# Kernel tuning notes

Measured on AMD Instinct MI355X. Metric: run time of the kernel, lower is better.

## Reference

```python
import jax, jax.numpy as jnp
import numpy as np

ALPHA = 0.1
BETA = 1.1
NUM_CLASSES = 16
EPS = 1e-8  # matches torch cosine_similarity eps
BATCH = 131072
DIM = 512


def setup_inputs() -> dict:
    key = jax.random.key(0)
    k1, k2 = jax.random.split(key)
    embeddings = jax.random.normal(k1, (BATCH, DIM), dtype=jnp.float32)
    labels = jax.random.randint(k2, (BATCH,), 0, NUM_CLASSES)
    return {"embeddings": embeddings, "labels": labels}


def _cos_dist(a, b):
    # a: [M, D], b: [N, D] -> 1 - cosine_similarity, shape [M, N]
    an = a / jnp.maximum(jnp.linalg.norm(a, axis=-1, keepdims=True), EPS)
    bn = b / jnp.maximum(jnp.linalg.norm(b, axis=-1, keepdims=True), EPS)
    return 1.0 - an @ bn.T


def reference(embeddings, labels):
    C = NUM_CLASSES
    N = embeddings.shape[0]
    dt = embeddings.dtype

    # class centroids (dummy anchors) via scatter-mean
    cnt = jax.ops.segment_sum(jnp.ones((N,), dt), labels, num_segments=C)  # [C]
    sums = jax.ops.segment_sum(embeddings, labels, num_segments=C)        # [C, D]
    centroids = sums / jnp.maximum(cnt, 1.0)[:, None]
    present = cnt > 0

    # close class pairs: i < j, both present, centroid distance <= beta
    pd = _cos_dist(centroids, centroids)                    # [C, C]
    upper = jnp.triu(jnp.ones((C, C), bool), k=1)
    pairmask = upper & (pd <= BETA) & present[:, None] & present[None, :]
    pm = pairmask.astype(dt)
    deg = pm.sum(1) + pm.sum(0)                             # pairs involving each class

    # distances from every centroid to every sample
    D = _cos_dist(centroids, embeddings)                    # [C, N]

    # intra: each sample of class c contributes relu(d(cent_c, x) - alpha),
    # once per close pair involving c
    d_own = D[labels, jnp.arange(N)]                        # [N]
    intra_sum = jnp.sum(deg[labels] * jax.nn.relu(d_own - ALPHA))

    # inter: S[c, c'] = sum over samples with label c' of relu(beta - d(cent_c, x))
    S = jax.ops.segment_sum(jax.nn.relu(BETA - D).T, labels, num_segments=C).T  # [C, C]
    inter_sum = jnp.sum(pm * (S + S.T))

    # number of terms in each loss list: sum over pairs of (cnt_i + cnt_j)
    count = jnp.sum(deg * cnt)
    denom = jnp.maximum(count, 1.0)
    num_pairs = pm.sum()

    loss = jnp.where(num_pairs > 0, intra_sum / denom + inter_sum / denom, 0.0)
    return loss
```

## Files before the change

### kernel.cpp

```cpp
#include <hip/hip_runtime.h>

constexpr float kAlpha = 0.1f;
constexpr float kBeta  = 1.1f;
constexpr int   kC     = 16;
constexpr int   kD     = 512;
constexpr float kEps   = 1e-8f;

constexpr int SUMS_OFF = 0;
constexpr int CNT_OFF  = 8192;
constexpr int TOT_OFF  = 8208;
constexpr int CTR1_OFF = 8209;
constexpr int CTR2_OFF = 8210;
constexpr int FLAG_OFF = 8224;
constexpr int PDM_OFF  = 8960;
constexpr int CN_OFF   = 9216;
constexpr int MSK_OFF  = 17408;
constexpr int SCL_OFF  = 17424;
constexpr int ZERO_FLOATS = 8211;

__device__ __forceinline__ float dot4(float4 a, float4 b) {
    return a.x * b.x + a.y * b.y + a.z * b.z + a.w * b.w;
}

__global__ __launch_bounds__(256) void k1_sums(const float* __restrict__ emb,
                                               const int* __restrict__ labels,
                                               float* __restrict__ ws,
                                               int N, int rpb) {
    __shared__ float lacc[kC * kD];
    float* sums  = ws + SUMS_OFF;
    float* cnt_g = ws + CNT_OFF;
    float* cn_g  = ws + CN_OFF;
    float* pdm_g = ws + PDM_OFF;
    float* scal  = ws + SCL_OFF;
    unsigned* mask_g = (unsigned*)(ws + MSK_OFF);
    int* ctr1 = (int*)(ws + CTR1_OFF);
    int* flag = (int*)(ws + FLAG_OFF);

    int tid = threadIdx.x;
    int wave = tid >> 6, lane = tid & 63;
    int half = wave & 1, strm = wave >> 1;

    for (int i = tid; i < kC * kD; i += 256) lacc[i] = 0.f;

    float4 acc[kC];
#pragma unroll
    for (int c = 0; c < kC; ++c) acc[c] = make_float4(0.f, 0.f, 0.f, 0.f);
    float cacc = 0.f;

    const float4* e4 = (const float4*)emb;
    int r0 = blockIdx.x * rpb;
    int r1 = min(r0 + rpb, N);
    const int o = half * 64 + lane;

    for (int base = r0 + strm; base < r1; base += 8) {
        int rA = base;
        int rB = base + 2, rC = base + 4, rD = base + 6;
        int cB = rB < r1 ? rB : rA;
        int cC = rC < r1 ? rC : rA;
        int cD = rD < r1 ? rD : rA;
        float4 xA = e4[(size_t)rA * 128 + o];
        float4 xB = e4[(size_t)cB * 128 + o];
        float4 xC = e4[(size_t)cC * 128 + o];
        float4 xD = e4[(size_t)cD * 128 + o];
        int laA = __builtin_amdgcn_readfirstlane(labels[rA]);
        int laB = rB < r1 ? __builtin_amdgcn_readfirstlane(labels[cB]) : -1;
        int laC = rC < r1 ? __builtin_amdgcn_readfirstlane(labels[cC]) : -1;
        int laD = rD < r1 ? __builtin_amdgcn_readfirstlane(labels[cD]) : -1;
#pragma unroll
        for (int c = 0; c < kC; ++c) {
            float mA = (laA == c) ? 1.f : 0.f;
            float mB = (laB == c) ? 1.f : 0.f;
            float mC = (laC == c) ? 1.f : 0.f;
            float mD = (laD == c) ? 1.f : 0.f;
            acc[c].x += mA * xA.x; acc[c].y += mA * xA.y; acc[c].z += mA * xA.z; acc[c].w += mA * xA.w;
            acc[c].x += mB * xB.x; acc[c].y += mB * xB.y; acc[c].z += mB * xB.z; acc[c].w += mB * xB.w;
            acc[c].x += mC * xC.x; acc[c].y += mC * xC.y; acc[c].z += mC * xC.z; acc[c].w += mC * xC.w;
            acc[c].x += mD * xD.x; acc[c].y += mD * xD.y; acc[c].z += mD * xD.z; acc[c].w += mD * xD.w;
        }
        if (half == 0) {
            cacc += ((laA == lane) ? 1.f : 0.f) + ((laB == lane) ? 1.f : 0.f)
                  + ((laC == lane) ? 1.f : 0.f) + ((laD == lane) ? 1.f : 0.f);
        }
    }

    __syncthreads();
#pragma unroll 1
    for (int s = 0; s < kC; ++s) {
        int c = (s + wave * 4) & 15;
        float* p = &lacc[c * kD + half * 256 + lane];
        float4 a = acc[c];
        p[0]   += a.x;
        p[64]  += a.y;
        p[128] += a.z;
        p[192] += a.w;
        __syncthreads();
    }

    for (int g = tid; g < kC * kD; g += 256) {
        int c = g >> 9, d = g & 511;
        int hh = d >> 8, u = d & 255;
        int l = u >> 2, k = u & 3;
        atomicAdd(&sums[g], lacc[c * kD + hh * 256 + k * 64 + l]);
    }
    if (half == 0 && lane < kC) atomicAdd(&cnt_g[lane], cacc);

    __threadfence();
    __syncthreads();
    if (tid == 0) {
        int old = atomicAdd(ctr1, 1);
        flag[blockIdx.x] = (old == (int)gridDim.x - 1) ? 1 : 0;
    }
    __syncthreads();
    if (flag[blockIdx.x] == 0) return;
    __threadfence();

    int c = tid >> 4, sub = tid & 15;
    float cntc = atomicAdd(&cnt_g[c], 0.f);
    float invc = 1.f / fmaxf(cntc, 1.f);
    float sq = 0.f;
    for (int d = sub; d < kD; d += 16) {
        float v = atomicAdd(&sums[c * kD + d], 0.f) * invc;
        lacc[c * kD + d] = v;
        sq += v * v;
    }
#pragma unroll
    for (int m = 1; m < 16; m <<= 1) sq += __shfl_xor(sq, m, 64);
    float inv = 1.f / fmaxf(sqrtf(sq), kEps);
    for (int d = sub; d < kD; d += 16) {
        float v = lacc[c * kD + d] * inv;
        lacc[c * kD + d] = v;
        cn_g[c * kD + d] = v;
    }
    __syncthreads();

    int pi = tid >> 4, pj = tid & 15;
    float dot = 0.f;
    for (int dd = 0; dd < kD; ++dd) {
        int d = (dd + tid) & (kD - 1);
        dot += lacc[pi * kD + d] * lacc[pj * kD + d];
    }
    pdm_g[tid] = 1.f - dot;
    __syncthreads();

    if (tid == 0) {
        float lc[kC];
        for (int a = 0; a < kC; ++a) lc[a] = atomicAdd(&cnt_g[a], 0.f);
        unsigned m[kC];
        for (int a = 0; a < kC; ++a) m[a] = 0u;
        float npairs = 0.f;
        for (int a = 0; a < kC; ++a)
            for (int b = a + 1; b < kC; ++b) {
                bool close = (pdm_g[a * kC + b] <= kBeta) && (lc[a] > 0.f) && (lc[b] > 0.f);
                if (close) { m[a] |= 1u << b; m[b] |= 1u << a; npairs += 1.f; }
            }
        float count = 0.f;
        for (int a = 0; a < kC; ++a) {
            mask_g[a] = m[a];
            count += (float)__popc(m[a]) * lc[a];
        }
        scal[0] = fmaxf(count, 1.f);
        scal[1] = npairs;
    }
}

__global__ __launch_bounds__(512, 2) void k3_main(const float* __restrict__ emb,
                                                  const int* __restrict__ labels,
                                                  float* __restrict__ ws,
                                                  float* __restrict__ out,
                                                  int N, int rpb) {
    __shared__ unsigned lmask[kC];
    __shared__ float wsum[8];
    const float* cn_g = ws + CN_OFF;
    const unsigned* mask_g = (const unsigned*)(ws + MSK_OFF);
    float* total = ws + TOT_OFF;
    const float* scal = ws + SCL_OFF;
    int* ctr2 = (int*)(ws + CTR2_OFF);

    int tid = threadIdx.x;
    int wave = tid >> 6, lane = tid & 63;
    int g = lane >> 4, j = lane & 15;

    const float4* w4 = (const float4*)cn_g;
    float4 wreg[4][8];
#pragma unroll
    for (int c = 0; c < 4; ++c)
#pragma unroll
        for (int i = 0; i < 8; ++i)
            wreg[c][i] = w4[(4 * g + c) * 128 + i * 16 + j];
    if (tid < kC) lmask[tid] = mask_g[tid];
    __syncthreads();

    int r0 = blockIdx.x * rpb;
    int r1 = min(r0 + rpb, N);
    const float4* src = (const float4*)emb;
    float priv = 0.f;

#define K3_COMPUTE(X, LAB)                                                     \
    do {                                                                       \
        float d0 = 0.f, d1 = 0.f, d2 = 0.f, d3 = 0.f, nrm = 0.f;               \
        _Pragma("unroll")                                                      \
        for (int i = 0; i < 8; ++i) {                                          \
            float4 x = X[i];                                                   \
            nrm += dot4(x, x);                                                 \
            d0 += dot4(x, wreg[0][i]);                                         \
            d1 += dot4(x, wreg[1][i]);                                         \
            d2 += dot4(x, wreg[2][i]);                                         \
            d3 += dot4(x, wreg[3][i]);                                         \
        }                                                                      \
        _Pragma("unroll")                                                      \
        for (int m = 1; m < 16; m <<= 1) {                                     \
            d0 += __shfl_xor(d0, m, 64);                                       \
            d1 += __shfl_xor(d1, m, 64);                                       \
            d2 += __shfl_xor(d2, m, 64);                                       \
            d3 += __shfl_xor(d3, m, 64);                                       \
            nrm += __shfl_xor(nrm, m, 64);                                     \
        }                                                                      \
        if (j == 0) {                                                          \
            unsigned mm = lmask[LAB];                                          \
            float inv = 1.f / fmaxf(sqrtf(nrm), kEps);                         \
            float dv[4] = {d0, d1, d2, d3};                                    \
            float s = 0.f;                                                     \
            _Pragma("unroll")                                                  \
            for (int c = 0; c < 4; ++c) {                                      \
                int cg = 4 * g + c;                                            \
                float dd = 1.f - dv[c] * inv;                                  \
                if ((mm >> cg) & 1u) s += fmaxf(kBeta - dd, 0.f);              \
                if (cg == LAB) s += (float)__popc(mm) * fmaxf(dd - kAlpha, 0.f);\
            }                                                                  \
            priv += s;                                                         \
        }                                                                      \
    } while (0)

    int rA = r0 + wave;
    if (rA < r1) {
        float4 xA[8], xB[8];
        int laA, laB;
#pragma unroll
        for (int i = 0; i < 8; ++i) xA[i] = src[(size_t)rA * 128 + i * 16 + j];
        laA = labels[rA];
        int rB = rA + 8;
        while (true) {
            bool vB = rB < r1;
            int rBi = vB ? rB : rA;
#pragma unroll
            for (int i = 0; i < 8; ++i) xB[i] = src[(size_t)rBi * 128 + i * 16 + j];
            laB = labels[rBi];
            K3_COMPUTE(xA, laA);
            if (!vB) break;

            int rN = rB + 8;
            bool vN = rN < r1;
            int rNi = vN ? rN : rB;
#pragma unroll
            for (int i = 0; i < 8; ++i) xA[i] = src[(size_t)rNi * 128 + i * 16 + j];
            laA = labels[rNi];
            K3_COMPUTE(xB, laB);
            if (!vN) break;
            rA = rN;
            rB = rN + 8;
        }
    }
#undef K3_COMPUTE

#pragma unroll
    for (int off = 32; off > 0; off >>= 1) priv += __shfl_down(priv, off, 64);
    if (lane == 0) wsum[wave] = priv;
    __syncthreads();
    if (tid == 0) {
        float t = 0.f;
#pragma unroll
        for (int w = 0; w < 8; ++w) t += wsum[w];
        atomicAdd(total, t);
        __threadfence();
        int old = atomicAdd(ctr2, 1);
        if (old == (int)gridDim.x - 1) {
            float tot = atomicAdd(total, 0.f);
            out[0] = (scal[1] > 0.f) ? (tot / scal[0]) : 0.f;
        }
    }
}

extern "C" void kernel_launch(void* const* d_in, const int* in_sizes, int n_in,
                              void* d_out, int out_size, void* d_ws, size_t ws_size,
                              hipStream_t stream) {
    const float* emb = (const float*)d_in[0];
    const int* labels = (const int*)d_in[1];
    int N = in_sizes[0] / kD;

    float* ws = (float*)d_ws;
    hipMemsetAsync(d_ws, 0, ZERO_FLOATS * sizeof(float), stream);

    int blocks1 = 512;
    int rpb1 = (N + blocks1 - 1) / blocks1;
    k1_sums<<<blocks1, 256, 0, stream>>>(emb, labels, ws, N, rpb1);

    int blocks3 = 256;
    int rpb3 = (N + blocks3 - 1) / blocks3;
    k3_main<<<blocks3, 512, 0, stream>>>(emb, labels, ws, (float*)d_out, N, rpb3);
}
```

Baseline: 559.0 us.

## Deepen load pipelining in both passes and double k1 block size

The centroid-sum kernel now runs 512 threads per block, and each wave loads 8 rows per iteration instead of 4, so more memory requests are in flight. The last-block flag moves from global memory into shared memory. The distance kernel switches from double buffering to a three-buffer rotation, keeping two row loads outstanding while one row is computed. The cost is higher register pressure, from the 16 float4 accumulators plus 8 row buffers in k1 and 24 float4 buffers in k3, which may limit occupancy.

Result: slower. 841.3 us (+50.5%).

```diff
diff --git a/kernel.cpp b/kernel.cpp
--- a/kernel.cpp
+++ b/kernel.cpp
@@ -11,7 +11,6 @@
 constexpr int TOT_OFF  = 8208;
 constexpr int CTR1_OFF = 8209;
 constexpr int CTR2_OFF = 8210;
-constexpr int FLAG_OFF = 8224;
 constexpr int PDM_OFF  = 8960;
 constexpr int CN_OFF   = 9216;
 constexpr int MSK_OFF  = 17408;
@@ -22,11 +21,12 @@
     return a.x * b.x + a.y * b.y + a.z * b.z + a.w * b.w;
 }
 
-__global__ __launch_bounds__(256) void k1_sums(const float* __restrict__ emb,
-                                               const int* __restrict__ labels,
-                                               float* __restrict__ ws,
-                                               int N, int rpb) {
+__global__ __launch_bounds__(512, 4) void k1_sums(const float* __restrict__ emb,
+                                                  const int* __restrict__ labels,
+                                                  float* __restrict__ ws,
+                                                  int N, int rpb) {
     __shared__ float lacc[kC * kD];
+    __shared__ int lastblk;
     float* sums  = ws + SUMS_OFF;
     float* cnt_g = ws + CNT_OFF;
     float* cn_g  = ws + CN_OFF;
@@ -34,13 +34,12 @@
     float* scal  = ws + SCL_OFF;
     unsigned* mask_g = (unsigned*)(ws + MSK_OFF);
     int* ctr1 = (int*)(ws + CTR1_OFF);
-    int* flag = (int*)(ws + FLAG_OFF);
 
     int tid = threadIdx.x;
     int wave = tid >> 6, lane = tid & 63;
     int half = wave & 1, strm = wave >> 1;
 
-    for (int i = tid; i < kC * kD; i += 256) lacc[i] = 0.f;
+    for (int i = tid; i < kC * kD; i += 512) lacc[i] = 0.f;
 
     float4 acc[kC];
 #pragma unroll
@@ -52,41 +51,41 @@
     int r1 = min(r0 + rpb, N);
     const int o = half * 64 + lane;
 
-    for (int base = r0 + strm; base < r1; base += 8) {
-        int rA = base;
-        int rB = base + 2, rC = base + 4, rD = base + 6;
-        int cB = rB < r1 ? rB : rA;
-        int cC = rC < r1 ? rC : rA;
-        int cD = rD < r1 ? rD : rA;
-        float4 xA = e4[(size_t)rA * 128 + o];
-        float4 xB = e4[(size_t)cB * 128 + o];
-        float4 xC = e4[(size_t)cC * 128 + o];
-        float4 xD = e4[(size_t)cD * 128 + o];
-        int laA = __builtin_amdgcn_readfirstlane(labels[rA]);
-        int laB = rB < r1 ? __builtin_amdgcn_readfirstlane(labels[cB]) : -1;
-        int laC = rC < r1 ? __builtin_amdgcn_readfirstlane(labels[cC]) : -1;
-        int laD = rD < r1 ? __builtin_amdgcn_readfirstlane(labels[cD]) : -1;
+    for (int base = r0 + strm; base < r1; base += 32) {
+        float4 xb[8];
+        int lab[8];
+#pragma unroll
+        for (int k = 0; k < 8; ++k) {
+            int rk = base + 4 * k;
+            bool vk = rk < r1;
+            int ck = vk ? rk : base;
+            xb[k] = e4[(size_t)ck * 128 + o];
+            int lv = labels[ck];
+            lab[k] = __builtin_amdgcn_readfirstlane(vk ? lv : -1);
+        }
 #pragma unroll
         for (int c = 0; c < kC; ++c) {
-            float mA = (laA == c) ? 1.f : 0.f;
-            float mB = (laB == c) ? 1.f : 0.f;
-            float mC = (laC == c) ? 1.f : 0.f;
-            float mD = (laD == c) ? 1.f : 0.f;
-            acc[c].x += mA * xA.x; acc[c].y += mA * xA.y; acc[c].z += mA * xA.z; acc[c].w += mA * xA.w;
-            acc[c].x += mB * xB.x; acc[c].y += mB * xB.y; acc[c].z += mB * xB.z; acc[c].w += mB * xB.w;
-            acc[c].x += mC * xC.x; acc[c].y += mC * xC.y; acc[c].z += mC * xC.z; acc[c].w += mC * xC.w;
-            acc[c].x += mD * xD.x; acc[c].y += mD * xD.y; acc[c].z += mD * xD.z; acc[c].w += mD * xD.w;
+            float4 a = acc[c];
+#pragma unroll
+            for (int k = 0; k < 8; ++k) {
+                float m = (lab[k] == c) ? 1.f : 0.f;
+                a.x += m * xb[k].x;
+                a.y += m * xb[k].y;
+                a.z += m * xb[k].z;
+                a.w += m * xb[k].w;
+            }
+            acc[c] = a;
         }
         if (half == 0) {
-            cacc += ((laA == lane) ? 1.f : 0.f) + ((laB == lane) ? 1.f : 0.f)
-                  + ((laC == lane) ? 1.f : 0.f) + ((laD == lane) ? 1.f : 0.f);
+#pragma unroll
+            for (int k = 0; k < 8; ++k) cacc += (lab[k] == lane) ? 1.f : 0.f;
         }
     }
 
     __syncthreads();
 #pragma unroll 1
     for (int s = 0; s < kC; ++s) {
-        int c = (s + wave * 4) & 15;
+        int c = (s + strm * 4) & 15;
         float* p = &lacc[c * kD + half * 256 + lane];
         float4 a = acc[c];
         p[0]   += a.x;
@@ -96,7 +95,7 @@
         __syncthreads();
     }
 
-    for (int g = tid; g < kC * kD; g += 256) {
+    for (int g = tid; g < kC * kD; g += 512) {
         int c = g >> 9, d = g & 511;
         int hh = d >> 8, u = d & 255;
         int l = u >> 2, k = u & 3;
@@ -108,38 +107,41 @@
     __syncthreads();
     if (tid == 0) {
         int old = atomicAdd(ctr1, 1);
-        flag[blockIdx.x] = (old == (int)gridDim.x - 1) ? 1 : 0;
-    }
-    __syncthreads();
-    if (flag[blockIdx.x] == 0) return;
+        lastblk = (old == (int)gridDim.x - 1) ? 1 : 0;
+    }
+    __syncthreads();
+    if (!lastblk) return;
     __threadfence();
 
-    int c = tid >> 4, sub = tid & 15;
-    float cntc = atomicAdd(&cnt_g[c], 0.f);
-    float invc = 1.f / fmaxf(cntc, 1.f);
-    float sq = 0.f;
-    for (int d = sub; d < kD; d += 16) {
-        float v = atomicAdd(&sums[c * kD + d], 0.f) * invc;
-        lacc[c * kD + d] = v;
-        sq += v * v;
-    }
-#pragma unroll
-    for (int m = 1; m < 16; m <<= 1) sq += __shfl_xor(sq, m, 64);
-    float inv = 1.f / fmaxf(sqrtf(sq), kEps);
-    for (int d = sub; d < kD; d += 16) {
-        float v = lacc[c * kD + d] * inv;
-        lacc[c * kD + d] = v;
-        cn_g[c * kD + d] = v;
-    }
-    __syncthreads();
-
-    int pi = tid >> 4, pj = tid & 15;
-    float dot = 0.f;
-    for (int dd = 0; dd < kD; ++dd) {
-        int d = (dd + tid) & (kD - 1);
-        dot += lacc[pi * kD + d] * lacc[pj * kD + d];
-    }
-    pdm_g[tid] = 1.f - dot;
+    int c2 = tid >> 4, sub = tid & 15;
+    if (tid < 256) {
+        float cntc = atomicAdd(&cnt_g[c2], 0.f);
+        float invc = 1.f / fmaxf(cntc, 1.f);
+        float sq = 0.f;
+        for (int d = sub; d < kD; d += 16) {
+            float v = atomicAdd(&sums[c2 * kD + d], 0.f) * invc;
+            lacc[c2 * kD + d] = v;
+            sq += v * v;
+        }
+#pragma unroll
+        for (int m = 1; m < 16; m <<= 1) sq += __shfl_xor(sq, m, 64);
+        float inv = 1.f / fmaxf(sqrtf(sq), kEps);
+        for (int d = sub; d < kD; d += 16) {
+            float v = lacc[c2 * kD + d] * inv;
+            lacc[c2 * kD + d] = v;
+            cn_g[c2 * kD + d] = v;
+        }
+    }
+    __syncthreads();
+    if (tid < 256) {
+        int pi = tid >> 4, pj = tid & 15;
+        float dot = 0.f;
+        for (int dd = 0; dd < kD; ++dd) {
+            int d = (dd + tid) & (kD - 1);
+            dot += lacc[pi * kD + d] * lacc[pj * kD + d];
+        }
+        pdm_g[tid] = 1.f - dot;
+    }
     __syncthreads();
 
     if (tid == 0) {
@@ -194,6 +196,14 @@
     int r1 = min(r0 + rpb, N);
     const float4* src = (const float4*)emb;
     float priv = 0.f;
+
+#define LOADX(B, L, ROW)                                                       \
+    do {                                                                       \
+        int _r = (ROW);                                                        \
+        _Pragma("unroll")                                                      \
+        for (int i = 0; i < 8; ++i) B[i] = src[(size_t)_r * 128 + i * 16 + j]; \
+        L = labels[_r];                                                        \
+    } while (0)
 
 #define K3_COMPUTE(X, LAB)                                                     \
     do {                                                                       \
@@ -231,36 +241,35 @@
         }                                                                      \
     } while (0)
 
-    int rA = r0 + wave;
-    if (rA < r1) {
-        float4 xA[8], xB[8];
-        int laA, laB;
-#pragma unroll
-        for (int i = 0; i < 8; ++i) xA[i] = src[(size_t)rA * 128 + i * 16 + j];
-        laA = labels[rA];
-        int rB = rA + 8;
+    int r = r0 + wave;
+    if (r < r1) {
+        float4 b0[8], b1[8], b2[8];
+        int l0, l1, l2;
+        LOADX(b0, l0, r);
+        bool v1 = (r + 8) < r1;
+        { int rr = v1 ? r + 8 : r; LOADX(b1, l1, rr); }
+        bool v2 = (r + 16) < r1;
+        { int rr = v2 ? r + 16 : r; LOADX(b2, l2, rr); }
         while (true) {
-            bool vB = rB < r1;
-            int rBi = vB ? rB : rA;
-#pragma unroll
-            for (int i = 0; i < 8; ++i) xB[i] = src[(size_t)rBi * 128 + i * 16 + j];
-            laB = labels[rBi];
-            K3_COMPUTE(xA, laA);
-            if (!vB) break;
-
-            int rN = rB + 8;
-            bool vN = rN < r1;
-            int rNi = vN ? rN : rB;
-#pragma unroll
-            for (int i = 0; i < 8; ++i) xA[i] = src[(size_t)rNi * 128 + i * 16 + j];
-            laA = labels[rNi];
-            K3_COMPUTE(xB, laB);
-            if (!vN) break;
-            rA = rN;
-            rB = rN + 8;
+            bool v3 = (r + 24) < r1;
+            K3_COMPUTE(b0, l0);
+            if (!v1) break;
+            { int rr = v3 ? r + 24 : r + 8; LOADX(b0, l0, rr); }
+            bool v4 = (r + 32) < r1;
+            K3_COMPUTE(b1, l1);
+            if (!v2) break;
+            { int rr = v4 ? r + 32 : r + 8; LOADX(b1, l1, rr); }
+            bool v5 = (r + 40) < r1;
+            K3_COMPUTE(b2, l2);
+            if (!v3) break;
+            { int rr = v5 ? r + 40 : r + 8; LOADX(b2, l2, rr); }
+            r += 24;
+            v1 = v4;
+            v2 = v5;
         }
     }
 #undef K3_COMPUTE
+#undef LOADX
 
 #pragma unroll
     for (int off = 32; off > 0; off >>= 1) priv += __shfl_down(priv, off, 64);
@@ -292,7 +301,7 @@
 
     int blocks1 = 512;
     int rpb1 = (N + blocks1 - 1) / blocks1;
-    k1_sums<<<blocks1, 256, 0, stream>>>(emb, labels, ws, N, rpb1);
+    k1_sums<<<blocks1, 512, 0, stream>>>(emb, labels, ws, N, rpb1);
 
     int blocks3 = 256;
     int rpb3 = (N + blocks3 - 1) / blocks3;
```
